# Kernel tuning notes

Measured on AMD Instinct MI355X. Metric: run time of the kernel, lower is better.

The kernel has to match this reference:

```python
import jax, jax.numpy as jnp
import numpy as np

EPS = 1e-7  # tf.keras.backend.epsilon()


def squash(v, axis=-1):
    s = jnp.sum(jnp.square(v), axis=axis, keepdims=True)
    scale = s / (1.0 + s) / jnp.sqrt(s + EPS)
    return scale * v


def setup_inputs() -> dict:
    key = jax.random.key(0)
    k1, k2 = jax.random.split(key)
    B, I, D = 64, 2048, 16   # batch, input_num_capsule, input_dim_capsule
    J, K = 32, 16            # num_capsule, dim_capsule
    inputs = jax.random.normal(k1, (B, I, D), dtype=jnp.float32)
    # glorot_uniform-ish init for W: [in_caps, num_caps, in_dim, dim_caps]
    limit = np.sqrt(6.0 / (D + K)).astype(np.float32)
    W = jax.random.uniform(k2, (I, J, D, K), dtype=jnp.float32, minval=-limit, maxval=limit)
    return {"inputs": inputs, "W": W}


def reference(inputs, W, routings=3):
    # u_hat[b,i,j,:] = inputs[b,i,:] @ W[i,j,:,:]
    u_hat = jnp.einsum('bid,ijdk->bijk', inputs, W)  # [B, I, J, K]
    B, I, J, _ = u_hat.shape
    b = jnp.zeros((B, I, J, 1), dtype=u_hat.dtype)
    outputs = None
    for r in range(routings):
        c = jax.nn.softmax(b, axis=2)                              # [B, I, J, 1]
        outputs = squash(jnp.sum(c * u_hat, axis=1, keepdims=True))  # [B, 1, J, K]
        if r < routings - 1:
            b = b + jnp.sum(u_hat * outputs, axis=-1, keepdims=True)
    return jnp.squeeze(outputs, axis=1)  # [B, J, K]
```

## Files before the change

### kernel.cpp

```cpp
#include <hip/hip_runtime.h>
#include <hip/hip_bf16.h>


#define B_ 64
#define I_ 2048
#define D_ 16
#define J_ 32
#define K_ 16
#define JK 512

typedef __attribute__((ext_vector_type(8))) short short8;
typedef __attribute__((ext_vector_type(4))) float float4v;

__device__ __forceinline__ unsigned short f2bf(float f) {
    union { float f; unsigned int i; } v;
    v.f = f;
    const unsigned int x = v.i;
    return (unsigned short)((x + 0x7fffu + ((x >> 16) & 1u)) >> 16);
}

__device__ __forceinline__ void unpack8(const uint4 r, float* u) {
    union { unsigned int i; float f; } t;
    t.i = r.x << 16;         u[0] = t.f;
    t.i = r.x & 0xffff0000u; u[1] = t.f;
    t.i = r.y << 16;         u[2] = t.f;
    t.i = r.y & 0xffff0000u; u[3] = t.f;
    t.i = r.z << 16;         u[4] = t.f;
    t.i = r.z & 0xffff0000u; u[5] = t.f;
    t.i = r.w << 16;         u[6] = t.f;
    t.i = r.w & 0xffff0000u; u[7] = t.f;
}

__global__ __launch_bounds__(256)
void caps_produce(const float* __restrict__ x, const float* __restrict__ W,
                  unsigned short* __restrict__ uhat) {
    __shared__ unsigned short wlds[32 * 384];
    __shared__ unsigned short zbuf[8];
    __shared__ unsigned short ctile[4][16 * 264];
    const int i = blockIdx.x;
    const int tid = threadIdx.x;

    if (tid < 8) zbuf[tid] = 0;

    {
        const float* wbase = W + (size_t)i * (J_ * D_ * K_);
        const int k = tid & 15;
#pragma unroll
        for (int half = 0; half < 2; ++half) {
            const int j = (tid >> 4) + half * 16;
            const float* p = wbase + j * (D_ * K_) + k;
            float vals[16];
#pragma unroll
            for (int d = 0; d < 16; ++d) vals[d] = p[d * K_];
            unsigned int pk[8];
#pragma unroll
            for (int q = 0; q < 8; ++q)
                pk[q] = ((unsigned int)f2bf(vals[2 * q + 1]) << 16) |
                        f2bf(vals[2 * q]);
            uint4* dst = reinterpret_cast<uint4*>(wlds + j * 384 + k * 24);
            uint4 w0; w0.x = pk[0]; w0.y = pk[1]; w0.z = pk[2]; w0.w = pk[3];
            uint4 w1; w1.x = pk[4]; w1.y = pk[5]; w1.z = pk[6]; w1.w = pk[7];
            dst[0] = w0; dst[1] = w1;
        }
    }
    __syncthreads();

    const int lane = tid & 63;
    const int wv = tid >> 6;
    const int quad = lane >> 4;
    const int l15 = lane & 15;
    const int b = wv * 16 + l15;

    union { uint4 u; short8 s; } bfrag;
    {
        const float* xp = x + ((size_t)b * I_ + i) * D_ + (quad & 1) * 8;
        const float4 x0 = reinterpret_cast<const float4*>(xp)[0];
        const float4 x1 = reinterpret_cast<const float4*>(xp)[1];
        bfrag.u.x = ((unsigned int)f2bf(x0.y) << 16) | f2bf(x0.x);
        bfrag.u.y = ((unsigned int)f2bf(x0.w) << 16) | f2bf(x0.z);
        bfrag.u.z = ((unsigned int)f2bf(x1.y) << 16) | f2bf(x1.x);
        bfrag.u.w = ((unsigned int)f2bf(x1.w) << 16) | f2bf(x1.z);
        if (quad >= 2) { bfrag.u.x = 0; bfrag.u.y = 0; bfrag.u.z = 0; bfrag.u.w = 0; }
    }

    const unsigned short* aptr =
        (quad >= 2) ? zbuf : (wlds + l15 * 24 + (quad & 1) * 8);
    const int astride = (quad >= 2) ? 0 : 384;
    unsigned short* ct = &ctile[wv][0];

    for (int jh = 0; jh < 2; ++jh) {
#pragma unroll
        for (int jj = 0; jj < 16; ++jj) {
            const int j = jh * 16 + jj;
            union { uint4 u; short8 s; } af;
            af.u = *reinterpret_cast<const uint4*>(aptr + (size_t)j * astride);
            float4v acc = {0.f, 0.f, 0.f, 0.f};
            acc = __builtin_amdgcn_mfma_f32_16x16x32_bf16(af.s, bfrag.s, acc,
                                                          0, 0, 0);
            uint2 pk;
            pk.x = ((unsigned int)f2bf(acc[1]) << 16) | f2bf(acc[0]);
            pk.y = ((unsigned int)f2bf(acc[3]) << 16) | f2bf(acc[2]);
            *reinterpret_cast<uint2*>(ct + l15 * 264 + jj * 16 + quad * 4) = pk;
        }
#pragma unroll
        for (int r = 0; r < 8; ++r) {
            const int bsub = r * 2 + (lane >> 5);
            const int c32 = lane & 31;
            const uint4 val = *reinterpret_cast<const uint4*>(
                ct + bsub * 264 + c32 * 8);
            *reinterpret_cast<uint4*>(
                uhat + ((size_t)(wv * 16 + bsub) * I_ + i) * JK + jh * 256 +
                c32 * 8) = val;
        }
    }
}

__global__ __launch_bounds__(256)
void caps_sum0(const unsigned short* __restrict__ uhat,
               float* __restrict__ spart2) {
    __shared__ float part[4][512];
    const int bq = blockIdx.x;
    const int b = bq >> 2, q = bq & 3;
    const int lane = threadIdx.x & 63;
    const int w = threadIdx.x >> 6;

    const unsigned short* up =
        uhat + ((size_t)b * I_ + q * 512 + w * 128) * JK + lane * 8;

    float acc[8];
#pragma unroll
    for (int k = 0; k < 8; ++k) acc[k] = 0.f;

    for (int ii = 0; ii < 128; ii += 4) {
        uint4 r[4];
#pragma unroll
        for (int s = 0; s < 4; ++s)
            r[s] = *reinterpret_cast<const uint4*>(up + (size_t)(ii + s) * JK);
#pragma unroll
        for (int s = 0; s < 4; ++s) {
            float u[8];
            unpack8(r[s], u);
#pragma unroll
            for (int k = 0; k < 8; ++k) acc[k] += u[k];
        }
    }

    float4 o0, o1;
    o0.x = acc[0]; o0.y = acc[1]; o0.z = acc[2]; o0.w = acc[3];
    o1.x = acc[4]; o1.y = acc[5]; o1.z = acc[6]; o1.w = acc[7];
    reinterpret_cast<float4*>(&part[w][lane * 8])[0] = o0;
    reinterpret_cast<float4*>(&part[w][lane * 8])[1] = o1;
    __syncthreads();

    const int t = threadIdx.x;
#pragma unroll
    for (int e = 0; e < 2; ++e) {
        const int jk = t * 2 + e;
        spart2[(size_t)bq * 512 + jk] =
            part[0][jk] + part[1][jk] + part[2][jk] + part[3][jk];
    }
}

__global__ __launch_bounds__(512)
void caps_squash0(const float* __restrict__ spart2, float* __restrict__ vsum) {
    const int bl = blockIdx.x;
    const int jk = threadIdx.x;
    float s = spart2[(size_t)(bl * 4 + 0) * 512 + jk] +
              spart2[(size_t)(bl * 4 + 1) * 512 + jk] +
              spart2[(size_t)(bl * 4 + 2) * 512 + jk] +
              spart2[(size_t)(bl * 4 + 3) * 512 + jk];
    s *= (1.f / 32.f);
    float q = s * s;
    q += __shfl_xor(q, 1, 64);
    q += __shfl_xor(q, 2, 64);
    q += __shfl_xor(q, 4, 64);
    q += __shfl_xor(q, 8, 64);
    const float scale = q / ((1.f + q) * sqrtf(q + 1e-7f));
    vsum[bl * JK + jk] = scale * s;
}

__global__ __launch_bounds__(64)
void caps_route1(const unsigned short* __restrict__ uhat,
                 const float* __restrict__ vsum, float* __restrict__ spart) {
    const int lane = threadIdx.x;
    const int bl = blockIdx.x >> 6;
    const int chunk = blockIdx.x & 63;
    const int h = lane >> 5;
    const int j = lane & 31;

    float v[16];
    {
        const float4* vp =
            reinterpret_cast<const float4*>(vsum + bl * JK + j * 16);
        const float4 a0 = vp[0], a1 = vp[1], a2 = vp[2], a3 = vp[3];
        v[0] = a0.x; v[1] = a0.y; v[2] = a0.z; v[3] = a0.w;
        v[4] = a1.x; v[5] = a1.y; v[6] = a1.z; v[7] = a1.w;
        v[8] = a2.x; v[9] = a2.y; v[10] = a2.z; v[11] = a2.w;
        v[12] = a3.x; v[13] = a3.y; v[14] = a3.z; v[15] = a3.w;
    }

    float acc[16];
#pragma unroll
    for (int k = 0; k < 16; ++k) acc[k] = 0.f;

    const unsigned short* up =
        uhat + ((size_t)bl * I_ + chunk * 32 + h) * JK + j * 16;

    uint4 c0 = reinterpret_cast<const uint4*>(up)[0];
    uint4 c1 = reinterpret_cast<const uint4*>(up)[1];

#pragma unroll 4
    for (int t = 0; t < 16; ++t) {
        uint4 n0, n1;
        if (t < 15) {
            const uint4* np =
                reinterpret_cast<const uint4*>(up + (size_t)(t + 1) * 2 * JK);
            n0 = np[0];
            n1 = np[1];
        }
        float u[16];
        unpack8(c0, u);
        unpack8(c1, u + 8);
        float p = 0.f;
#pragma unroll
        for (int k = 0; k < 16; ++k) p += u[k] * v[k];
        const float e = __expf(p);
        float S = e;
        S += __shfl_xor(S, 1, 64);
        S += __shfl_xor(S, 2, 64);
        S += __shfl_xor(S, 4, 64);
        S += __shfl_xor(S, 8, 64);
        S += __shfl_xor(S, 16, 64);
        const float c = e / S;
#pragma unroll
        for (int k = 0; k < 16; ++k) acc[k] += c * u[k];
        c0 = n0;
        c1 = n1;
    }

#pragma unroll
    for (int k = 0; k < 16; ++k) acc[k] += __shfl_xor(acc[k], 32, 64);

    if (h == 0) {
        float* sp = spart + ((size_t)chunk * B_ + bl) * JK + j * 16;
#pragma unroll
        for (int q = 0; q < 4; ++q) {
            float4 o;
            o.x = acc[q * 4 + 0]; o.y = acc[q * 4 + 1];
            o.z = acc[q * 4 + 2]; o.w = acc[q * 4 + 3];
            reinterpret_cast<float4*>(sp)[q] = o;
        }
    }
}

template <int MODE>
__global__ __launch_bounds__(512)
void caps_squash(const float* __restrict__ spart, float* __restrict__ vsum,
                 float* __restrict__ out) {
    const int bl = blockIdx.x;
    const int jk = threadIdx.x;
    float s = 0.f;
#pragma unroll 8
    for (int p = 0; p < 64; ++p)
        s += spart[((size_t)p * B_ + bl) * JK + jk];
    float q = s * s;
    q += __shfl_xor(q, 1, 64);
    q += __shfl_xor(q, 2, 64);
    q += __shfl_xor(q, 4, 64);
    q += __shfl_xor(q, 8, 64);
    const float scale = q / ((1.f + q) * sqrtf(q + 1e-7f));
    const float v = scale * s;
    if (MODE == 1) vsum[bl * JK + jk] += v;
    else           out[(size_t)bl * JK + jk] = v;
}

extern "C" void kernel_launch(void* const* d_in, const int* in_sizes, int n_in,
                              void* d_out, int out_size, void* d_ws,
                              size_t ws_size, hipStream_t stream) {
    const float* x = (const float*)d_in[0];
    const float* W = (const float*)d_in[1];
    float* out = (float*)d_out;

    char* ws = (char*)d_ws;
    unsigned short* uhat = (unsigned short*)ws;
    float* spart = (float*)(ws + (size_t)B_ * I_ * JK * 2);
    float* vsum = spart + (size_t)64 * B_ * JK;

    caps_produce<<<I_, 256, 0, stream>>>(x, W, uhat);

    caps_sum0<<<256, 256, 0, stream>>>(uhat, spart);
    caps_squash0<<<B_, 512, 0, stream>>>(spart, vsum);

    caps_route1<<<4096, 64, 0, stream>>>(uhat, vsum, spart);
    caps_squash<1><<<B_, 512, 0, stream>>>(spart, vsum, out);

    caps_route1<<<4096, 64, 0, stream>>>(uhat, vsum, spart);
    caps_squash<2><<<B_, 512, 0, stream>>>(spart, vsum, out);
}
```

Before: 202.1 us.

## Deepen uhat prefetch, shrink LDS tile, overlap x load with W staging

In the producer kernel the x fragment load now happens before W is staged into LDS, and the output staging tile is shrunk to 8 capsules per group with four groups, which cuts LDS use and may allow more blocks per CU. The routing kernel replaces its single-step prefetch with a four-deep register ring buffer of uhat loads and fully unrolls the loop. The softmax division is replaced by a hardware reciprocal multiply. This raises register pressure and slightly reduces division precision.

```diff
diff --git a/kernel.cpp b/kernel.cpp
--- a/kernel.cpp
+++ b/kernel.cpp
@@ -36,34 +36,11 @@
                   unsigned short* __restrict__ uhat) {
     __shared__ unsigned short wlds[32 * 384];
     __shared__ unsigned short zbuf[8];
-    __shared__ unsigned short ctile[4][16 * 264];
+    __shared__ unsigned short ctile[4][16 * 136];
     const int i = blockIdx.x;
     const int tid = threadIdx.x;
 
     if (tid < 8) zbuf[tid] = 0;
-
-    {
-        const float* wbase = W + (size_t)i * (J_ * D_ * K_);
-        const int k = tid & 15;
-#pragma unroll
-        for (int half = 0; half < 2; ++half) {
-            const int j = (tid >> 4) + half * 16;
-            const float* p = wbase + j * (D_ * K_) + k;
-            float vals[16];
-#pragma unroll
-            for (int d = 0; d < 16; ++d) vals[d] = p[d * K_];
-            unsigned int pk[8];
-#pragma unroll
-            for (int q = 0; q < 8; ++q)
-                pk[q] = ((unsigned int)f2bf(vals[2 * q + 1]) << 16) |
-                        f2bf(vals[2 * q]);
-            uint4* dst = reinterpret_cast<uint4*>(wlds + j * 384 + k * 24);
-            uint4 w0; w0.x = pk[0]; w0.y = pk[1]; w0.z = pk[2]; w0.w = pk[3];
-            uint4 w1; w1.x = pk[4]; w1.y = pk[5]; w1.z = pk[6]; w1.w = pk[7];
-            dst[0] = w0; dst[1] = w1;
-        }
-    }
-    __syncthreads();
 
     const int lane = tid & 63;
     const int wv = tid >> 6;
@@ -83,15 +60,38 @@
         if (quad >= 2) { bfrag.u.x = 0; bfrag.u.y = 0; bfrag.u.z = 0; bfrag.u.w = 0; }
     }
 
+    {
+        const float* wbase = W + (size_t)i * (J_ * D_ * K_);
+        const int k = tid & 15;
+#pragma unroll
+        for (int half = 0; half < 2; ++half) {
+            const int j = (tid >> 4) + half * 16;
+            const float* p = wbase + j * (D_ * K_) + k;
+            float vals[16];
+#pragma unroll
+            for (int d = 0; d < 16; ++d) vals[d] = p[d * K_];
+            unsigned int pk[8];
+#pragma unroll
+            for (int q = 0; q < 8; ++q)
+                pk[q] = ((unsigned int)f2bf(vals[2 * q + 1]) << 16) |
+                        f2bf(vals[2 * q]);
+            uint4* dst = reinterpret_cast<uint4*>(wlds + j * 384 + k * 24);
+            uint4 w0; w0.x = pk[0]; w0.y = pk[1]; w0.z = pk[2]; w0.w = pk[3];
+            uint4 w1; w1.x = pk[4]; w1.y = pk[5]; w1.z = pk[6]; w1.w = pk[7];
+            dst[0] = w0; dst[1] = w1;
+        }
+    }
+    __syncthreads();
+
     const unsigned short* aptr =
         (quad >= 2) ? zbuf : (wlds + l15 * 24 + (quad & 1) * 8);
     const int astride = (quad >= 2) ? 0 : 384;
     unsigned short* ct = &ctile[wv][0];
 
-    for (int jh = 0; jh < 2; ++jh) {
-#pragma unroll
-        for (int jj = 0; jj < 16; ++jj) {
-            const int j = jh * 16 + jj;
+    for (int jg = 0; jg < 4; ++jg) {
+#pragma unroll
+        for (int jj = 0; jj < 8; ++jj) {
+            const int j = jg * 8 + jj;
             union { uint4 u; short8 s; } af;
             af.u = *reinterpret_cast<const uint4*>(aptr + (size_t)j * astride);
             float4v acc = {0.f, 0.f, 0.f, 0.f};
@@ -100,17 +100,17 @@
             uint2 pk;
             pk.x = ((unsigned int)f2bf(acc[1]) << 16) | f2bf(acc[0]);
             pk.y = ((unsigned int)f2bf(acc[3]) << 16) | f2bf(acc[2]);
-            *reinterpret_cast<uint2*>(ct + l15 * 264 + jj * 16 + quad * 4) = pk;
-        }
-#pragma unroll
-        for (int r = 0; r < 8; ++r) {
-            const int bsub = r * 2 + (lane >> 5);
-            const int c32 = lane & 31;
+            *reinterpret_cast<uint2*>(ct + l15 * 136 + jj * 16 + quad * 4) = pk;
+        }
+#pragma unroll
+        for (int r = 0; r < 4; ++r) {
+            const int bsub = r * 4 + (lane >> 4);
+            const int c16 = lane & 15;
             const uint4 val = *reinterpret_cast<const uint4*>(
-                ct + bsub * 264 + c32 * 8);
+                ct + bsub * 136 + c16 * 8);
             *reinterpret_cast<uint4*>(
-                uhat + ((size_t)(wv * 16 + bsub) * I_ + i) * JK + jh * 256 +
-                c32 * 8) = val;
+                uhat + ((size_t)(wv * 16 + bsub) * I_ + i) * JK + jg * 128 +
+                c16 * 8) = val;
         }
     }
 }
@@ -206,21 +206,26 @@
     const unsigned short* up =
         uhat + ((size_t)bl * I_ + chunk * 32 + h) * JK + j * 16;
 
-    uint4 c0 = reinterpret_cast<const uint4*>(up)[0];
-    uint4 c1 = reinterpret_cast<const uint4*>(up)[1];
-
-#pragma unroll 4
+    uint4 pf[4][2];
+#pragma unroll
+    for (int s = 0; s < 4; ++s) {
+        const uint4* p = reinterpret_cast<const uint4*>(up + (size_t)s * 2 * JK);
+        pf[s][0] = p[0];
+        pf[s][1] = p[1];
+    }
+
+#pragma unroll
     for (int t = 0; t < 16; ++t) {
-        uint4 n0, n1;
-        if (t < 15) {
-            const uint4* np =
-                reinterpret_cast<const uint4*>(up + (size_t)(t + 1) * 2 * JK);
-            n0 = np[0];
-            n1 = np[1];
-        }
+        const int slot = t & 3;
         float u[16];
-        unpack8(c0, u);
-        unpack8(c1, u + 8);
+        unpack8(pf[slot][0], u);
+        unpack8(pf[slot][1], u + 8);
+        if (t + 4 < 16) {
+            const uint4* p =
+                reinterpret_cast<const uint4*>(up + (size_t)(t + 4) * 2 * JK);
+            pf[slot][0] = p[0];
+            pf[slot][1] = p[1];
+        }
         float p = 0.f;
 #pragma unroll
         for (int k = 0; k < 16; ++k) p += u[k] * v[k];
@@ -231,11 +236,9 @@
         S += __shfl_xor(S, 4, 64);
         S += __shfl_xor(S, 8, 64);
         S += __shfl_xor(S, 16, 64);
-        const float c = e / S;
+        const float c = e * __builtin_amdgcn_rcpf(S);
 #pragma unroll
         for (int k = 0; k < 16; ++k) acc[k] += c * u[k];
-        c0 = n0;
-        c1 = n1;
     }
 
 #pragma unroll
```

After: 230.3 us. 13.9% more time.
